# Optimization experiments

Hardware: AMD Instinct MI355X
Metric: run time of the kernel (lower is better)

Reference implementation:

```python
import jax, jax.numpy as jnp
import numpy as np

N_NODES = 100000
N_EDGES = 3200000
D_IN = 256
D_OUT = 256


def setup_inputs() -> dict:
    key = jax.random.key(0)
    k1, k2, k3, k4, k5, k6 = jax.random.split(key, 6)
    x = jax.random.normal(k1, (N_NODES, D_IN), dtype=jnp.float32)
    edge_row = jax.random.randint(k2, (N_EDGES,), 0, N_NODES, dtype=jnp.int32)
    edge_col = jax.random.randint(k3, (N_EDGES,), 0, N_NODES, dtype=jnp.int32)
    edge_val = jax.random.uniform(k4, (N_EDGES,), dtype=jnp.float32)
    # nn.Linear params (PyTorch stores weight as [out, in]; we apply x @ W.T + b)
    bound = 1.0 / np.sqrt(D_IN)
    W = jax.random.uniform(k5, (D_OUT, D_IN), minval=-bound, maxval=bound, dtype=jnp.float32)
    b = jax.random.uniform(k6, (D_OUT,), minval=-bound, maxval=bound, dtype=jnp.float32)
    return {"x": x, "edge_row": edge_row, "edge_col": edge_col,
            "edge_val": edge_val, "W": W, "b": b}


def reference(x, edge_row, edge_col, edge_val, W, b):
    # SpMM: agg[i] = sum over edges e with row[e]==i of val[e] * x[col[e]]
    messages = edge_val[:, None] * x[edge_col]          # [E, D_in]
    agg = jax.ops.segment_sum(messages, edge_row, num_segments=N_NODES)  # [N, D_in]
    # Dense linear: agg @ W.T + b
    return jnp.einsum('nd,od->no', agg, W) + b
```

## Files before the change

### kernel.cpp

```cpp
#include <hip/hip_runtime.h>

#define THREADS 256

typedef __attribute__((ext_vector_type(8))) short short8;
typedef __attribute__((ext_vector_type(4))) float f32x4;

__device__ __forceinline__ unsigned short f2bf(float f) {
    unsigned u = __builtin_bit_cast(unsigned, f);
    return (unsigned short)((u + 0x7FFFu + ((u >> 16) & 1u)) >> 16);
}
__device__ __forceinline__ float bf2f_lo(unsigned u) { return __builtin_bit_cast(float, u << 16); }
__device__ __forceinline__ float bf2f_hi(unsigned u) { return __builtin_bit_cast(float, u & 0xFFFF0000u); }

#define P1B 1024

__global__ void fusedA_kernel(const int* __restrict__ row, const int* __restrict__ col,
                              const float* __restrict__ val, int* __restrict__ gcur,
                              uint2* __restrict__ estage,
                              const float* __restrict__ W, unsigned short* __restrict__ WbP,
                              const float4* __restrict__ x, uint4* __restrict__ xb,
                              int n_edges, int nbkt, int capB, int n8) {
    int b = blockIdx.x, tid = threadIdx.x;
    if (b < P1B) {
        __shared__ int h[512];
        __shared__ int curl[512];
        int E0 = (int)((long long)b * n_edges / P1B);
        int E1 = (int)((long long)(b + 1) * n_edges / P1B);
        for (int i = tid; i < 512; i += THREADS) h[i] = 0;
        __syncthreads();
        for (int e = E0 + tid; e < E1; e += THREADS)
            atomicAdd(&h[row[e] >> 8], 1);
        __syncthreads();
        for (int bk = tid; bk < nbkt; bk += THREADS) {
            int c = h[bk];
            curl[bk] = bk * capB + (c ? atomicAdd(&gcur[bk], c) : 0);
        }
        __syncthreads();
        for (int e = E0 + tid; e < E1; e += THREADS) {
            int r = row[e];
            int bk = r >> 8;
            int pos = atomicAdd(&curl[bk], 1);
            if (pos < (bk + 1) * capB)
                estage[pos] = make_uint2(((unsigned)(r & 255) << 24) | (unsigned)col[e],
                                         (unsigned)__float_as_int(val[e]));
        }
    } else if (b < P1B + 32) {
        int f = (b - P1B) * THREADS + tid;
        int l = f & 63, nt = (f >> 6) & 15, k0i = f >> 10;
        int r = nt * 16 + (l & 15);
        int koff = k0i * 32 + 8 * (l >> 4);
        const float4* s = reinterpret_cast<const float4*>(W + r * 256 + koff);
        float4 a = s[0], bb = s[1];
        uint4 o;
        o.x = (unsigned)f2bf(a.x) | ((unsigned)f2bf(a.y) << 16);
        o.y = (unsigned)f2bf(a.z) | ((unsigned)f2bf(a.w) << 16);
        o.z = (unsigned)f2bf(bb.x) | ((unsigned)f2bf(bb.y) << 16);
        o.w = (unsigned)f2bf(bb.z) | ((unsigned)f2bf(bb.w) << 16);
        reinterpret_cast<uint4*>(WbP)[f] = o;
    } else {
        int i = (b - P1B - 32) * THREADS + tid;
        if (i >= n8) return;
        float4 a = x[2 * i], bb = x[2 * i + 1];
        uint4 o;
        o.x = (unsigned)f2bf(a.x) | ((unsigned)f2bf(a.y) << 16);
        o.y = (unsigned)f2bf(a.z) | ((unsigned)f2bf(a.w) << 16);
        o.z = (unsigned)f2bf(bb.x) | ((unsigned)f2bf(bb.y) << 16);
        o.w = (unsigned)f2bf(bb.z) | ((unsigned)f2bf(bb.w) << 16);
        reinterpret_cast<uint4*>(xb)[i] = o;
    }
}

__global__ void p2_sort(const uint2* __restrict__ estage, const int* __restrict__ gcur,
                        int2* __restrict__ pr, int* __restrict__ offs,
                        int capB, int n_nodes, int nbkt) {
    __shared__ int red[256];
    __shared__ int h[256];
    __shared__ int curh[256];
    __shared__ int wsum[4];
    int b = blockIdx.x, tid = threadIdx.x;

    int partial = 0;
    for (int j = tid; j < b; j += THREADS) {
        int c = gcur[j];
        partial += c > capB ? capB : c;
    }
    red[tid] = partial;
    __syncthreads();
    #pragma unroll
    for (int s = 128; s > 0; s >>= 1) {
        if (tid < s) red[tid] += red[tid + s];
        __syncthreads();
    }
    int gb = red[0];
    int count = gcur[b]; if (count > capB) count = capB;
    int base = b * capB;

    h[tid] = 0;
    __syncthreads();
    for (int i = tid; i < count; i += THREADS)
        atomicAdd(&h[estage[base + i].x >> 24], 1);
    __syncthreads();
    int v = h[tid];
    int lane = tid & 63, w = tid >> 6;
    int incl = v;
    #pragma unroll
    for (int off = 1; off < 64; off <<= 1) {
        int t = __shfl_up(incl, off, 64);
        if (lane >= off) incl += t;
    }
    if (lane == 63) wsum[w] = incl;
    __syncthreads();
    int wo = 0;
    for (int i = 0; i < w; ++i) wo += wsum[i];
    int excl = wo + incl - v;
    int node = b * 256 + tid;
    if (node < n_nodes) offs[node] = gb + excl;
    curh[tid] = gb + excl;
    if (b == nbkt - 1 && tid == 0) offs[n_nodes] = gb + count;
    __syncthreads();
    for (int i = tid; i < count; i += THREADS) {
        uint2 p = estage[base + i];
        int q = atomicAdd(&curh[(int)(p.x >> 24)], 1);
        pr[q] = make_int2((int)(p.x & 0x00FFFFFFu), (int)p.y);
    }
}

template<int OUT_BF16>
__global__ void spmm_bf16_kernel(const uint2* __restrict__ xb, const int* __restrict__ offs,
                                 const int2* __restrict__ pr, void* __restrict__ outp,
                                 int nnodes) {
    int wid = (blockIdx.x * blockDim.x + threadIdx.x) >> 6;
    int lane = threadIdx.x & 63;
    if (wid >= nnodes) return;
    int s = offs[wid], e = offs[wid + 1];
    float a0 = 0.f, a1 = 0.f, a2 = 0.f, a3 = 0.f;
    int i = s;
    if (i < e && (i & 1)) {
        int2 p = pr[i];
        uint2 xv = xb[(size_t)p.x * 64 + lane];
        float v = __int_as_float(p.y);
        a0 = fmaf(v, bf2f_lo(xv.x), a0); a1 = fmaf(v, bf2f_hi(xv.x), a1);
        a2 = fmaf(v, bf2f_lo(xv.y), a2); a3 = fmaf(v, bf2f_hi(xv.y), a3);
        ++i;
    }
    for (; i + 8 <= e; i += 8) {
        int4 pa = *reinterpret_cast<const int4*>(pr + i);
        int4 pb = *reinterpret_cast<const int4*>(pr + i + 2);
        int4 pc = *reinterpret_cast<const int4*>(pr + i + 4);
        int4 pd = *reinterpret_cast<const int4*>(pr + i + 6);
        uint2 x0 = xb[(size_t)pa.x * 64 + lane];
        uint2 x1 = xb[(size_t)pa.z * 64 + lane];
        uint2 x2 = xb[(size_t)pb.x * 64 + lane];
        uint2 x3 = xb[(size_t)pb.z * 64 + lane];
        uint2 x4_ = xb[(size_t)pc.x * 64 + lane];
        uint2 x5 = xb[(size_t)pc.z * 64 + lane];
        uint2 x6 = xb[(size_t)pd.x * 64 + lane];
        uint2 x7 = xb[(size_t)pd.z * 64 + lane];
        float v0 = __int_as_float(pa.y), v1 = __int_as_float(pa.w);
        float v2 = __int_as_float(pb.y), v3 = __int_as_float(pb.w);
        float v4 = __int_as_float(pc.y), v5 = __int_as_float(pc.w);
        float v6 = __int_as_float(pd.y), v7 = __int_as_float(pd.w);
        a0 = fmaf(v0, bf2f_lo(x0.x), a0); a1 = fmaf(v0, bf2f_hi(x0.x), a1);
        a2 = fmaf(v0, bf2f_lo(x0.y), a2); a3 = fmaf(v0, bf2f_hi(x0.y), a3);
        a0 = fmaf(v1, bf2f_lo(x1.x), a0); a1 = fmaf(v1, bf2f_hi(x1.x), a1);
        a2 = fmaf(v1, bf2f_lo(x1.y), a2); a3 = fmaf(v1, bf2f_hi(x1.y), a3);
        a0 = fmaf(v2, bf2f_lo(x2.x), a0); a1 = fmaf(v2, bf2f_hi(x2.x), a1);
        a2 = fmaf(v2, bf2f_lo(x2.y), a2); a3 = fmaf(v2, bf2f_hi(x2.y), a3);
        a0 = fmaf(v3, bf2f_lo(x3.x), a0); a1 = fmaf(v3, bf2f_hi(x3.x), a1);
        a2 = fmaf(v3, bf2f_lo(x3.y), a2); a3 = fmaf(v3, bf2f_hi(x3.y), a3);
        a0 = fmaf(v4, bf2f_lo(x4_.x), a0); a1 = fmaf(v4, bf2f_hi(x4_.x), a1);
        a2 = fmaf(v4, bf2f_lo(x4_.y), a2); a3 = fmaf(v4, bf2f_hi(x4_.y), a3);
        a0 = fmaf(v5, bf2f_lo(x5.x), a0); a1 = fmaf(v5, bf2f_hi(x5.x), a1);
        a2 = fmaf(v5, bf2f_lo(x5.y), a2); a3 = fmaf(v5, bf2f_hi(x5.y), a3);
        a0 = fmaf(v6, bf2f_lo(x6.x), a0); a1 = fmaf(v6, bf2f_hi(x6.x), a1);
        a2 = fmaf(v6, bf2f_lo(x6.y), a2); a3 = fmaf(v6, bf2f_hi(x6.y), a3);
        a0 = fmaf(v7, bf2f_lo(x7.x), a0); a1 = fmaf(v7, bf2f_hi(x7.x), a1);
        a2 = fmaf(v7, bf2f_lo(x7.y), a2); a3 = fmaf(v7, bf2f_hi(x7.y), a3);
    }
    for (; i + 2 <= e; i += 2) {
        int4 pa = *reinterpret_cast<const int4*>(pr + i);
        uint2 x0 = xb[(size_t)pa.x * 64 + lane];
        uint2 x1 = xb[(size_t)pa.z * 64 + lane];
        float v0 = __int_as_float(pa.y), v1 = __int_as_float(pa.w);
        a0 = fmaf(v0, bf2f_lo(x0.x), a0); a1 = fmaf(v0, bf2f_hi(x0.x), a1);
        a2 = fmaf(v0, bf2f_lo(x0.y), a2); a3 = fmaf(v0, bf2f_hi(x0.y), a3);
        a0 = fmaf(v1, bf2f_lo(x1.x), a0); a1 = fmaf(v1, bf2f_hi(x1.x), a1);
        a2 = fmaf(v1, bf2f_lo(x1.y), a2); a3 = fmaf(v1, bf2f_hi(x1.y), a3);
    }
    for (; i < e; ++i) {
        int2 p = pr[i];
        uint2 xv = xb[(size_t)p.x * 64 + lane];
        float v = __int_as_float(p.y);
        a0 = fmaf(v, bf2f_lo(xv.x), a0); a1 = fmaf(v, bf2f_hi(xv.x), a1);
        a2 = fmaf(v, bf2f_lo(xv.y), a2); a3 = fmaf(v, bf2f_hi(xv.y), a3);
    }
    if (OUT_BF16) {
        ushort4 o;
        o.x = f2bf(a0); o.y = f2bf(a1); o.z = f2bf(a2); o.w = f2bf(a3);
        *reinterpret_cast<ushort4*>((unsigned short*)outp + (size_t)wid * 256 + 4 * lane) = o;
    } else {
        ((float4*)outp)[(size_t)wid * 64 + lane] = make_float4(a0, a1, a2, a3);
    }
}

__global__ void spmm_f32_kernel(const float4* __restrict__ x4, const int* __restrict__ offs,
                                const int2* __restrict__ pr, float4* __restrict__ out4,
                                int nnodes) {
    int wid = (blockIdx.x * blockDim.x + threadIdx.x) >> 6;
    int lane = threadIdx.x & 63;
    if (wid >= nnodes) return;
    int s = offs[wid], e = offs[wid + 1];
    float4 acc = make_float4(0.f, 0.f, 0.f, 0.f);
    for (int i = s; i < e; ++i) {
        int2 p = pr[i];
        float4 xv = x4[(size_t)p.x * 64 + lane];
        float v = __int_as_float(p.y);
        acc.x = fmaf(v, xv.x, acc.x); acc.y = fmaf(v, xv.y, acc.y);
        acc.z = fmaf(v, xv.z, acc.z); acc.w = fmaf(v, xv.w, acc.w);
    }
    out4[(size_t)wid * 64 + lane] = acc;
}

__launch_bounds__(256)
__global__ void gemm_direct2_kernel(const unsigned short* __restrict__ aggb,
                                    const unsigned short* __restrict__ WbP,
                                    const float* __restrict__ bias,
                                    float* __restrict__ out, int n) {
    int tid = threadIdx.x, lane = tid & 63, w = tid >> 6;
    int row0 = blockIdx.x * 128 + w * 32;
    int lr = lane & 15, lg = lane >> 4;
    const unsigned short* arow0 = aggb + (size_t)(row0 + lr) * 256 + lg * 8;
    const unsigned short* arow1 = arow0 + 16 * 256;
    f32x4 acc0[16], acc1[16];
    #pragma unroll
    for (int nt = 0; nt < 16; ++nt) {
        acc0[nt] = (f32x4){0.f, 0.f, 0.f, 0.f};
        acc1[nt] = (f32x4){0.f, 0.f, 0.f, 0.f};
    }
    #pragma unroll
    for (int k = 0; k < 8; ++k) {
        short8 af0 = *reinterpret_cast<const short8*>(arow0 + k * 32);
        short8 af1 = *reinterpret_cast<const short8*>(arow1 + k * 32);
        #pragma unroll
        for (int nt = 0; nt < 16; ++nt) {
            short8 bf_ = *reinterpret_cast<const short8*>(
                &WbP[(size_t)((k * 16 + nt) * 64 + lane) * 8]);
            acc0[nt] = __builtin_amdgcn_mfma_f32_16x16x32_bf16(af0, bf_, acc0[nt], 0, 0, 0);
            acc1[nt] = __builtin_amdgcn_mfma_f32_16x16x32_bf16(af1, bf_, acc1[nt], 0, 0, 0);
        }
    }
    #pragma unroll
    for (int nt = 0; nt < 16; ++nt) {
        int gc = nt * 16 + lr;
        float bv = bias[gc];
        #pragma unroll
        for (int q = 0; q < 4; ++q) {
            int gr0 = row0 + lg * 4 + q;
            int gr1 = gr0 + 16;
            if (gr0 < n) out[(size_t)gr0 * 256 + gc] = acc0[nt][q] + bv;
            if (gr1 < n) out[(size_t)gr1 * 256 + gc] = acc1[nt][q] + bv;
        }
    }
}


__global__ void zero_kernel(int* __restrict__ p, int n) {
    int i = blockIdx.x * blockDim.x + threadIdx.x;
    if (i < n) p[i] = 0;
}

__global__ void hist_part_kernel(const int* __restrict__ row, int* __restrict__ cnt,
                                 int n_edges, int n_nodes) {
    int g = blockIdx.x & 7;
    int inst = blockIdx.x >> 3;
    int ninst = gridDim.x >> 3;
    int lo = (int)(((long long)g * n_nodes) >> 3);
    int hi = (int)(((long long)(g + 1) * n_nodes) >> 3);
    int e0 = (int)(((long long)inst * n_edges) / ninst);
    int e1 = (int)(((long long)(inst + 1) * n_edges) / ninst);
    for (int e = e0 + threadIdx.x; e < e1; e += THREADS) {
        int r = row[e];
        if (r >= lo && r < hi) atomicAdd(&cnt[r], 1);
    }
}

__global__ void place_part_kernel(const int* __restrict__ row, const int* __restrict__ col,
                                  const float* __restrict__ val, int* __restrict__ cur,
                                  int2* __restrict__ pr, int n_edges, int n_nodes) {
    int g = blockIdx.x & 7;
    int inst = blockIdx.x >> 3;
    int ninst = gridDim.x >> 3;
    int lo = (int)(((long long)g * n_nodes) >> 3);
    int hi = (int)(((long long)(g + 1) * n_nodes) >> 3);
    int e0 = (int)(((long long)inst * n_edges) / ninst);
    int e1 = (int)(((long long)(inst + 1) * n_edges) / ninst);
    for (int e = e0 + threadIdx.x; e < e1; e += THREADS) {
        int r = row[e];
        if (r >= lo && r < hi) {
            int p = atomicAdd(&cur[r], 1);
            pr[p] = make_int2(col[e], __float_as_int(val[e]));
        }
    }
}

__global__ void scan1_kernel(const int* __restrict__ cnt, int* __restrict__ offs,
                             int* __restrict__ bsum, int n) {
    int tid = threadIdx.x;
    int base = blockIdx.x * 1024 + tid * 4;
    int v0 = 0, v1 = 0, v2 = 0, v3 = 0;
    if (base + 3 < n) {
        int4 v = *reinterpret_cast<const int4*>(cnt + base);
        v0 = v.x; v1 = v.y; v2 = v.z; v3 = v.w;
    } else {
        if (base + 0 < n) v0 = cnt[base + 0];
        if (base + 1 < n) v1 = cnt[base + 1];
        if (base + 2 < n) v2 = cnt[base + 2];
    }
    int ts = v0 + v1 + v2 + v3;
    int lane = tid & 63;
    int incl = ts;
    #pragma unroll
    for (int off = 1; off < 64; off <<= 1) {
        int t = __shfl_up(incl, off, 64);
        if (lane >= off) incl += t;
    }
    __shared__ int wsum[4];
    int w = tid >> 6;
    if (lane == 63) wsum[w] = incl;
    __syncthreads();
    int wo = 0;
    for (int i = 0; i < w; ++i) wo += wsum[i];
    int excl = wo + incl - ts;
    if (base + 0 < n) offs[base + 0] = excl;
    if (base + 1 < n) offs[base + 1] = excl + v0;
    if (base + 2 < n) offs[base + 2] = excl + v0 + v1;
    if (base + 3 < n) offs[base + 3] = excl + v0 + v1 + v2;
    if (tid == THREADS - 1) bsum[blockIdx.x] = wo + incl;
}

__global__ void scan2_kernel(int* __restrict__ bsum, int nb) {
    int tid = threadIdx.x;
    int base = tid * 4;
    int v0 = 0, v1 = 0, v2 = 0, v3 = 0;
    if (base + 0 < nb) v0 = bsum[base + 0];
    if (base + 1 < nb) v1 = bsum[base + 1];
    if (base + 2 < nb) v2 = bsum[base + 2];
    if (base + 3 < nb) v3 = bsum[base + 3];
    int ts = v0 + v1 + v2 + v3;
    int lane = tid & 63;
    int incl = ts;
    #pragma unroll
    for (int off = 1; off < 64; off <<= 1) {
        int t = __shfl_up(incl, off, 64);
        if (lane >= off) incl += t;
    }
    __shared__ int wsum[4];
    int w = tid >> 6;
    if (lane == 63) wsum[w] = incl;
    __syncthreads();
    int wo = 0;
    for (int i = 0; i < w; ++i) wo += wsum[i];
    int excl = wo + incl - ts;
    if (base + 0 < nb) bsum[base + 0] = excl;
    if (base + 1 < nb) bsum[base + 1] = excl + v0;
    if (base + 2 < nb) bsum[base + 2] = excl + v0 + v1;
    if (base + 3 < nb) bsum[base + 3] = excl + v0 + v1 + v2;
    if (tid == THREADS - 1) bsum[nb] = wo + incl;
}

__global__ void scan3_kernel(int* __restrict__ offs, const int* __restrict__ bsum,
                             int* __restrict__ cur, int n) {
    int i = blockIdx.x * blockDim.x + threadIdx.x;
    if (i < n) {
        int v = offs[i] + bsum[i >> 10];
        offs[i] = v;
        cur[i] = v;
    }
    if (i == 0) offs[n] = bsum[(n + 1023) >> 10];
}

__global__ void cvt_bf16_kernel(const float4* __restrict__ in, uint4* __restrict__ out, int n8) {
    int i = blockIdx.x * blockDim.x + threadIdx.x;
    if (i >= n8) return;
    float4 a = in[2 * i], b = in[2 * i + 1];
    uint4 o;
    o.x = (unsigned)f2bf(a.x) | ((unsigned)f2bf(a.y) << 16);
    o.y = (unsigned)f2bf(a.z) | ((unsigned)f2bf(a.w) << 16);
    o.z = (unsigned)f2bf(b.x) | ((unsigned)f2bf(b.y) << 16);
    o.w = (unsigned)f2bf(b.z) | ((unsigned)f2bf(b.w) << 16);
    out[i] = o;
}

__launch_bounds__(256, 2)
__global__ void gemm_mfma_kernel(float* __restrict__ out, const unsigned short* __restrict__ Wb,
                                 const float* __restrict__ bias, int nrows) {
    __shared__ unsigned short As[64][264];
    __shared__ unsigned short Ws[256][40];
    int tid = threadIdx.x;
    int rowBase = blockIdx.x * 64;

    const float4* o4 = reinterpret_cast<const float4*>(out);
    for (int it = tid; it < 64 * 64; it += 256) {
        int r = it >> 6, c = it & 63;
        float4 v = make_float4(0.f, 0.f, 0.f, 0.f);
        int gr = rowBase + r;
        if (gr < nrows) v = o4[(size_t)gr * 64 + c];
        ushort4 w;
        w.x = f2bf(v.x); w.y = f2bf(v.y); w.z = f2bf(v.z); w.w = f2bf(v.w);
        *reinterpret_cast<ushort4*>(&As[r][c * 4]) = w;
    }

    int w = tid >> 6, lane = tid & 63;
    int lr = lane & 15, lg = lane >> 4;
    f32x4 acc[16];
    #pragma unroll
    for (int nt = 0; nt < 16; ++nt) acc[nt] = (f32x4){0.f, 0.f, 0.f, 0.f};

    for (int k0 = 0; k0 < 256; k0 += 32) {
        __syncthreads();
        for (int it = tid; it < 1024; it += 256) {
            int r = it >> 2, c = it & 3;
            uint4 v = *reinterpret_cast<const uint4*>(Wb + (size_t)r * 256 + k0 + c * 8);
            *reinterpret_cast<uint4*>(&Ws[r][c * 8]) = v;
        }
        __syncthreads();
        short8 af = *reinterpret_cast<const short8*>(&As[w * 16 + lr][k0 + 8 * lg]);
        #pragma unroll
        for (int nt = 0; nt < 16; ++nt) {
            short8 bf_ = *reinterpret_cast<const short8*>(&Ws[nt * 16 + lr][8 * lg]);
            acc[nt] = __builtin_amdgcn_mfma_f32_16x16x32_bf16(af, bf_, acc[nt], 0, 0, 0);
        }
    }

    #pragma unroll
    for (int nt = 0; nt < 16; ++nt) {
        int gc = nt * 16 + lr;
        float bv = bias[gc];
        #pragma unroll
        for (int q = 0; q < 4; ++q) {
            int gr = rowBase + w * 16 + lg * 4 + q;
            if (gr < nrows) out[(size_t)gr * 256 + gc] = acc[nt][q] + bv;
        }
    }
}


extern "C" void kernel_launch(void* const* d_in, const int* in_sizes, int n_in,
                              void* d_out, int out_size, void* d_ws, size_t ws_size,
                              hipStream_t stream) {
    const float* x     = (const float*)d_in[0];
    const int*   erow  = (const int*)d_in[1];
    const int*   ecol  = (const int*)d_in[2];
    const float* evalv = (const float*)d_in[3];
    const float* W     = (const float*)d_in[4];
    const float* bias  = (const float*)d_in[5];
    float* out = (float*)d_out;

    int n_nodes = in_sizes[0] / 256;
    int n_edges = in_sizes[1];

    int nbkt = (n_nodes + 255) >> 8;
    int avg = n_edges / (nbkt > 0 ? nbkt : 1);
    int capB = avg + avg / 4 + 1024;

    size_t A = (size_t)((n_nodes + 63) & ~63) + 64;
    int* offs  = (int*)d_ws;
    int* gcur  = offs + A;
    unsigned short* WbP = (unsigned short*)(gcur + 512);
    int2* pr = (int2*)(WbP + 65536);
    int* after_pr = (int*)(pr + n_edges);

    size_t est_ints  = (size_t)nbkt * capB * 2;
    size_t aggb_ints = (size_t)n_nodes * 128 + 32768;
    size_t xb_ints   = (size_t)n_nodes * 128;
    size_t alias_ints = est_ints > aggb_ints ? est_ints : aggb_ints;
    size_t head_ints = (size_t)(after_pr - (int*)d_ws);
    size_t need_new = (head_ints + alias_ints + xb_ints) * 4;
    bool new_ok = (nbkt <= 512) && (nbkt >= 1) && (n_nodes <= (1 << 24)) && ws_size >= need_new;

    if (new_ok) {
        uint2* estage = (uint2*)after_pr;
        unsigned short* aggb = (unsigned short*)after_pr;
        unsigned short* xb = (unsigned short*)(after_pr + alias_ints);

        hipMemsetAsync(gcur, 0, 512 * sizeof(int), stream);
        int n8 = n_nodes * 32;
        int cvtx_blocks = (n8 + THREADS - 1) / THREADS;
        fusedA_kernel<<<P1B + 32 + cvtx_blocks, THREADS, 0, stream>>>(
            erow, ecol, evalv, gcur, estage, W, WbP, (const float4*)x, (uint4*)xb,
            n_edges, nbkt, capB, n8);
        p2_sort<<<nbkt, THREADS, 0, stream>>>(estage, gcur, pr, offs, capB, n_nodes, nbkt);

        int spmm_blocks = (n_nodes + 3) / 4;
        spmm_bf16_kernel<1><<<spmm_blocks, THREADS, 0, stream>>>(
            (const uint2*)xb, offs, pr, aggb, n_nodes);
        int gb2 = (n_nodes + 127) / 128;
        gemm_direct2_kernel<<<gb2, THREADS, 0, stream>>>(aggb, WbP, bias, out, n_nodes);
    } else {
        int nb = (n_nodes + 1023) >> 10;
        size_t Af = (size_t)((n_nodes + 63) & ~63);
        int* cnt   = (int*)d_ws;
        int* offsf = cnt + Af;
        int* cur   = offsf + Af;
        int* bsum  = cur + Af;
        int* wbase = bsum + (((size_t)nb + 64) & ~63ull);
        unsigned short* Wbf = (unsigned short*)wbase;
        int2* prf  = (int2*)(Wbf + 65536);
        int* aft   = (int*)(prf + n_edges);
        unsigned short* xbf = (unsigned short*)aft;
        size_t need_old = (size_t)((char*)(xbf + (size_t)n_nodes * 256) - (char*)d_ws);
        bool told = ws_size >= need_old;

        zero_kernel<<<(n_nodes + THREADS - 1) / THREADS, THREADS, 0, stream>>>(cnt, n_nodes);
        hist_part_kernel<<<2048, THREADS, 0, stream>>>(erow, cnt, n_edges, n_nodes);
        scan1_kernel<<<nb, THREADS, 0, stream>>>(cnt, offsf, bsum, n_nodes);
        scan2_kernel<<<1, THREADS, 0, stream>>>(bsum, nb);
        scan3_kernel<<<(n_nodes + THREADS - 1) / THREADS, THREADS, 0, stream>>>(offsf, bsum, cur, n_nodes);
        place_part_kernel<<<2048, THREADS, 0, stream>>>(erow, ecol, evalv, cur, prf, n_edges, n_nodes);
        cvt_bf16_kernel<<<32, THREADS, 0, stream>>>((const float4*)W, (uint4*)Wbf, 65536 / 8);

        int gb = (n_nodes + 63) / 64;
        if (told) {
            int n8 = n_nodes * 32;
            cvt_bf16_kernel<<<(n8 + THREADS - 1) / THREADS, THREADS, 0, stream>>>(
                (const float4*)x, (uint4*)xbf, n8);
            int spmm_blocks = (n_nodes + 3) / 4;
            spmm_bf16_kernel<0><<<spmm_blocks, THREADS, 0, stream>>>(
                (const uint2*)xbf, offsf, prf, out, n_nodes);
        } else {
            int spmm_blocks = (n_nodes + 3) / 4;
            spmm_f32_kernel<<<spmm_blocks, THREADS, 0, stream>>>(
                (const float4*)x, offsf, prf, (float4*)out, n_nodes);
        }
        gemm_mfma_kernel<<<gb, THREADS, 0, stream>>>(out, Wbf, bias, n_nodes);
    }
}
```

Baseline: 455.6 us.

## Swizzle SpMM block-to-node mapping across XCDs and split GEMM output into halves

The SpMM kernel now remaps block indices so that consecutive blocks, which the hardware distributes round-robin over the 8 XCDs, cover different 256-node buckets. Each XCD therefore walks a contiguous set of buckets, which is meant to improve L2 locality on the sorted edge and offset arrays. The GEMM kernel preloads all A fragments into registers and computes the 256 output columns in two halves of 8 tiles. This halves the live accumulator registers and may raise occupancy, at the cost of holding the A fragments for the whole kernel. The launch grid is padded to a multiple of 8 buckets, so some blocks exit early.

```diff
diff --git a/kernel.cpp b/kernel.cpp
--- a/kernel.cpp
+++ b/kernel.cpp
@@ -129,7 +129,10 @@
 __global__ void spmm_bf16_kernel(const uint2* __restrict__ xb, const int* __restrict__ offs,
                                  const int2* __restrict__ pr, void* __restrict__ outp,
                                  int nnodes) {
-    int wid = (blockIdx.x * blockDim.x + threadIdx.x) >> 6;
+    int g = blockIdx.x & 7;
+    int inst = blockIdx.x >> 3;
+    int bkt = g + 8 * (inst >> 6);
+    int wid = bkt * 256 + (inst & 63) * 4 + (threadIdx.x >> 6);
     int lane = threadIdx.x & 63;
     if (wid >= nnodes) return;
     int s = offs[wid], e = offs[wid + 1];
@@ -222,7 +225,7 @@
 }
 
 __launch_bounds__(256)
-__global__ void gemm_direct2_kernel(const unsigned short* __restrict__ aggb,
+__global__ void gemm_direct3_kernel(const unsigned short* __restrict__ aggb,
                                     const unsigned short* __restrict__ WbP,
                                     const float* __restrict__ bias,
                                     float* __restrict__ out, int n) {
@@ -231,34 +234,41 @@
     int lr = lane & 15, lg = lane >> 4;
     const unsigned short* arow0 = aggb + (size_t)(row0 + lr) * 256 + lg * 8;
     const unsigned short* arow1 = arow0 + 16 * 256;
-    f32x4 acc0[16], acc1[16];
-    #pragma unroll
-    for (int nt = 0; nt < 16; ++nt) {
-        acc0[nt] = (f32x4){0.f, 0.f, 0.f, 0.f};
-        acc1[nt] = (f32x4){0.f, 0.f, 0.f, 0.f};
-    }
+    short8 af0[8], af1[8];
     #pragma unroll
     for (int k = 0; k < 8; ++k) {
-        short8 af0 = *reinterpret_cast<const short8*>(arow0 + k * 32);
-        short8 af1 = *reinterpret_cast<const short8*>(arow1 + k * 32);
+        af0[k] = *reinterpret_cast<const short8*>(arow0 + k * 32);
+        af1[k] = *reinterpret_cast<const short8*>(arow1 + k * 32);
+    }
+    #pragma unroll
+    for (int half = 0; half < 2; ++half) {
+        f32x4 acc0[8], acc1[8];
         #pragma unroll
-        for (int nt = 0; nt < 16; ++nt) {
-            short8 bf_ = *reinterpret_cast<const short8*>(
-                &WbP[(size_t)((k * 16 + nt) * 64 + lane) * 8]);
-            acc0[nt] = __builtin_amdgcn_mfma_f32_16x16x32_bf16(af0, bf_, acc0[nt], 0, 0, 0);
-            acc1[nt] = __builtin_amdgcn_mfma_f32_16x16x32_bf16(af1, bf_, acc1[nt], 0, 0, 0);
-        }
-    }
-    #pragma unroll
-    for (int nt = 0; nt < 16; ++nt) {
-        int gc = nt * 16 + lr;
-        float bv = bias[gc];
+        for (int nt = 0; nt < 8; ++nt) {
+            acc0[nt] = (f32x4){0.f, 0.f, 0.f, 0.f};
+            acc1[nt] = (f32x4){0.f, 0.f, 0.f, 0.f};
+        }
         #pragma unroll
-        for (int q = 0; q < 4; ++q) {
-            int gr0 = row0 + lg * 4 + q;
-            int gr1 = gr0 + 16;
-            if (gr0 < n) out[(size_t)gr0 * 256 + gc] = acc0[nt][q] + bv;
-            if (gr1 < n) out[(size_t)gr1 * 256 + gc] = acc1[nt][q] + bv;
+        for (int k = 0; k < 8; ++k) {
+            #pragma unroll
+            for (int nt = 0; nt < 8; ++nt) {
+                short8 bf_ = *reinterpret_cast<const short8*>(
+                    &WbP[(size_t)((k * 16 + half * 8 + nt) * 64 + lane) * 8]);
+                acc0[nt] = __builtin_amdgcn_mfma_f32_16x16x32_bf16(af0[k], bf_, acc0[nt], 0, 0, 0);
+                acc1[nt] = __builtin_amdgcn_mfma_f32_16x16x32_bf16(af1[k], bf_, acc1[nt], 0, 0, 0);
+            }
+        }
+        #pragma unroll
+        for (int nt = 0; nt < 8; ++nt) {
+            int gc = half * 128 + nt * 16 + lr;
+            float bv = bias[gc];
+            #pragma unroll
+            for (int q = 0; q < 4; ++q) {
+                int gr0 = row0 + lg * 4 + q;
+                int gr1 = gr0 + 16;
+                if (gr0 < n) out[(size_t)gr0 * 256 + gc] = acc0[nt][q] + bv;
+                if (gr1 < n) out[(size_t)gr1 * 256 + gc] = acc1[nt][q] + bv;
+            }
         }
     }
 }
@@ -491,11 +501,11 @@
             n_edges, nbkt, capB, n8);
         p2_sort<<<nbkt, THREADS, 0, stream>>>(estage, gcur, pr, offs, capB, n_nodes, nbkt);
 
-        int spmm_blocks = (n_nodes + 3) / 4;
+        int spmm_blocks = 8 * ((nbkt + 7) / 8) * 64;
         spmm_bf16_kernel<1><<<spmm_blocks, THREADS, 0, stream>>>(
             (const uint2*)xb, offs, pr, aggb, n_nodes);
-        int gb2 = (n_nodes + 127) / 128;
-        gemm_direct2_kernel<<<gb2, THREADS, 0, stream>>>(aggb, WbP, bias, out, n_nodes);
+        int gb = (n_nodes + 127) / 128;
+        gemm_direct3_kernel<<<gb, THREADS, 0, stream>>>(aggb, WbP, bias, out, n_nodes);
     } else {
         int nb = (n_nodes + 1023) >> 10;
         size_t Af = (size_t)((n_nodes + 63) & ~63);
@@ -524,12 +534,13 @@
             int n8 = n_nodes * 32;
             cvt_bf16_kernel<<<(n8 + THREADS - 1) / THREADS, THREADS, 0, stream>>>(
                 (const float4*)x, (uint4*)xbf, n8);
-            int spmm_blocks = (n_nodes + 3) / 4;
-            spmm_bf16_kernel<0><<<spmm_blocks, THREADS, 0, stream>>>(
+            int spmm_blocks_f = (n_nodes + 3) / 4;
+            spmm_bf16_kernel<0><<<8 * (((n_nodes + 255) / 256 + 7) / 8) * 64, THREADS, 0, stream>>>(
                 (const uint2*)xbf, offsf, prf, out, n_nodes);
+            (void)spmm_blocks_f;
         } else {
-            int spmm_blocks = (n_nodes + 3) / 4;
-            spmm_f32_kernel<<<spmm_blocks, THREADS, 0, stream>>>(
+            int spmm_blocks_f = (n_nodes + 3) / 4;
+            spmm_f32_kernel<<<spmm_blocks_f, THREADS, 0, stream>>>(
                 (const float4*)x, offsf, prf, (float4*)out, n_nodes);
         }
         gemm_mfma_kernel<<<gb, THREADS, 0, stream>>>(out, Wbf, bias, n_nodes);
```

New measurement: 422.9 us. 7.2% less time.
